# Kernel tuning notes

Hardware: AMD Instinct MI355X
Metric: run time of the kernel (lower is better)

The kernel has to match this reference:

```python
import jax, jax.numpy as jnp
import numpy as np

VEC_DIM = 300
NUM_DOCS = 500000
NUM_WORDS = 100000
BATCH = 4096
NUM_CTX = 10
NUM_NOISE_P1 = 26


def setup_inputs() -> dict:
    key = jax.random.key(0)
    k1, k2, k3, k4, k5 = jax.random.split(key, 5)
    context_ids = jax.random.randint(k1, (BATCH, NUM_CTX), 0, NUM_WORDS)
    doc_ids = jax.random.randint(k2, (BATCH,), 0, NUM_DOCS)
    target_noise_ids = jax.random.randint(k3, (BATCH, NUM_NOISE_P1), 0, NUM_WORDS)
    D = jax.random.normal(k4, (NUM_DOCS, VEC_DIM), dtype=jnp.float32)
    W = jax.random.normal(k5, (NUM_WORDS, VEC_DIM), dtype=jnp.float32)
    O = jnp.zeros((VEC_DIM, NUM_WORDS), dtype=jnp.float32)
    return {
        "context_ids": context_ids,
        "doc_ids": doc_ids,
        "target_noise_ids": target_noise_ids,
        "D": D,
        "W": W,
        "O": O,
    }


def reference(context_ids, doc_ids, target_noise_ids, D, W, O):
    # x[b] = D[doc_ids[b]] + sum_c W[context_ids[b, c]]   -> (B, vec_dim)
    x = D[doc_ids] + jnp.sum(W[context_ids], axis=1)
    # O[:, target_noise_ids] gathered as O.T[target_noise_ids] -> (B, N, vec_dim)
    # scores[b, n] = x[b] . O[:, target_noise_ids[b, n]]
    scores = jnp.einsum("bd,bnd->bn", x, O.T[target_noise_ids])
    return scores
```

## Files before the change

### kernel.cpp

```cpp
#include <hip/hip_runtime.h>

#define VEC_DIM   300
#define NUM_WORDS 100000
#define BATCH_N   4096
#define NUM_CTX   10
#define NUM_NOISE 26
#define TILE      64

__global__ __launch_bounds__(256) void transpose_kernel(
    const float* __restrict__ O,
    float*       __restrict__ OT)
{
    __shared__ float tile[TILE][TILE + 1];
    const int wBase = blockIdx.x * TILE;
    const int dBase = blockIdx.y * TILE;
    const int tx = threadIdx.x & (TILE - 1);
    const int ty = threadIdx.x >> 6;

    const int w_in = wBase + tx;
#pragma unroll
    for (int j = 0; j < TILE; j += 4) {
        const int d = dBase + ty + j;
        if (d < VEC_DIM && w_in < NUM_WORDS)
            tile[ty + j][tx] = O[(size_t)d * NUM_WORDS + w_in];
    }
    __syncthreads();

    const int d_out = dBase + tx;
#pragma unroll
    for (int j = 0; j < TILE; j += 4) {
        const int w = wBase + ty + j;
        if (w < NUM_WORDS && d_out < VEC_DIM)
            OT[(size_t)w * VEC_DIM + d_out] = tile[tx][ty + j];
    }
}

__global__ __launch_bounds__(256) void pvdm_score_kernel(
    const int*   __restrict__ context_ids,
    const int*   __restrict__ doc_ids,
    const int*   __restrict__ tn_ids,
    const float* __restrict__ D,
    const float* __restrict__ W,
    const float* __restrict__ OT,
    float*       __restrict__ out)
{
    __shared__ float xs[VEC_DIM];
    const int b   = blockIdx.x;
    const int tid = threadIdx.x;

    const int doc = doc_ids[b];
    int ctx[NUM_CTX];
#pragma unroll
    for (int c = 0; c < NUM_CTX; ++c) ctx[c] = context_ids[b * NUM_CTX + c];

    for (int d = tid; d < VEC_DIM; d += 256) {
        float v = D[(size_t)doc * VEC_DIM + d];
#pragma unroll
        for (int c = 0; c < NUM_CTX; ++c)
            v += W[(size_t)ctx[c] * VEC_DIM + d];
        xs[d] = v;
    }
    __syncthreads();

    const int wave = tid >> 6;
    const int lane = tid & 63;
    for (int n = wave; n < NUM_NOISE; n += 4) {
        const int t = tn_ids[b * NUM_NOISE + n];
        const float* row = OT + (size_t)t * VEC_DIM;
        float s = 0.0f;
        for (int d = lane; d < VEC_DIM; d += 64)
            s += xs[d] * row[d];
#pragma unroll
        for (int off = 32; off > 0; off >>= 1)
            s += __shfl_down(s, off, 64);
        if (lane == 0) out[b * NUM_NOISE + n] = s;
    }
}

__global__ __launch_bounds__(256) void pvdm_score_direct_kernel(
    const int*   __restrict__ context_ids,
    const int*   __restrict__ doc_ids,
    const int*   __restrict__ tn_ids,
    const float* __restrict__ D,
    const float* __restrict__ W,
    const float* __restrict__ O,
    float*       __restrict__ out)
{
    __shared__ float xs[VEC_DIM];
    const int b   = blockIdx.x;
    const int tid = threadIdx.x;
    const int doc = doc_ids[b];
    int ctx[NUM_CTX];
#pragma unroll
    for (int c = 0; c < NUM_CTX; ++c) ctx[c] = context_ids[b * NUM_CTX + c];
    for (int d = tid; d < VEC_DIM; d += 256) {
        float v = D[(size_t)doc * VEC_DIM + d];
#pragma unroll
        for (int c = 0; c < NUM_CTX; ++c)
            v += W[(size_t)ctx[c] * VEC_DIM + d];
        xs[d] = v;
    }
    __syncthreads();
    const int wave = tid >> 6;
    const int lane = tid & 63;
    for (int n = wave; n < NUM_NOISE; n += 4) {
        const int t = tn_ids[b * NUM_NOISE + n];
        float s = 0.0f;
        for (int d = lane; d < VEC_DIM; d += 64)
            s += xs[d] * O[(size_t)d * NUM_WORDS + t];
#pragma unroll
        for (int off = 32; off > 0; off >>= 1)
            s += __shfl_down(s, off, 64);
        if (lane == 0) out[b * NUM_NOISE + n] = s;
    }
}

extern "C" void kernel_launch(void* const* d_in, const int* in_sizes, int n_in,
                              void* d_out, int out_size, void* d_ws, size_t ws_size,
                              hipStream_t stream) {
    const int*   context_ids = (const int*)  d_in[0];
    const int*   doc_ids     = (const int*)  d_in[1];
    const int*   tn_ids      = (const int*)  d_in[2];
    const float* D           = (const float*)d_in[3];
    const float* W           = (const float*)d_in[4];
    const float* O           = (const float*)d_in[5];
    float*       out         = (float*)d_out;

    const size_t OT_BYTES = (size_t)NUM_WORDS * VEC_DIM * sizeof(float);

    if (ws_size >= OT_BYTES) {
        float* OT = (float*)d_ws;
        dim3 tgrid((NUM_WORDS + TILE - 1) / TILE, (VEC_DIM + TILE - 1) / TILE);
        transpose_kernel<<<tgrid, 256, 0, stream>>>(O, OT);
        pvdm_score_kernel<<<BATCH_N, 256, 0, stream>>>(
            context_ids, doc_ids, tn_ids, D, W, OT, out);
    } else {
        pvdm_score_direct_kernel<<<BATCH_N, 256, 0, stream>>>(
            context_ids, doc_ids, tn_ids, D, W, O, out);
    }
}
```

Measured before the change: 840.5 us.

## Vectorize transpose with full-row tiles and float4 score gathers

Rewrites the O transpose to load 32-word by full-dimension tiles with float4 reads and write whole contiguous OT rows with float4 stores. The score kernel now builds x with float4 loads using 75 threads and computes each dot product with float4 row reads, holding x in registers per lane. The aim is to cut transaction count and improve coalescing in the memory-bound transpose and gather. The larger shared tile reduces occupancy, and the strided shared-memory scatter may cause bank conflicts.

```diff
diff --git a/kernel.cpp b/kernel.cpp
--- a/kernel.cpp
+++ b/kernel.cpp
@@ -1,37 +1,38 @@
 #include <hip/hip_runtime.h>
 
 #define VEC_DIM   300
+#define VEC_F4    75
 #define NUM_WORDS 100000
 #define BATCH_N   4096
 #define NUM_CTX   10
 #define NUM_NOISE 26
-#define TILE      64
+#define TWORDS    32
 
 __global__ __launch_bounds__(256) void transpose_kernel(
     const float* __restrict__ O,
     float*       __restrict__ OT)
 {
-    __shared__ float tile[TILE][TILE + 1];
-    const int wBase = blockIdx.x * TILE;
-    const int dBase = blockIdx.y * TILE;
-    const int tx = threadIdx.x & (TILE - 1);
-    const int ty = threadIdx.x >> 6;
+    __shared__ float tile[TWORDS * VEC_DIM];
+    const int wBase = blockIdx.x * TWORDS;
+    const int tid   = threadIdx.x;
 
-    const int w_in = wBase + tx;
-#pragma unroll
-    for (int j = 0; j < TILE; j += 4) {
-        const int d = dBase + ty + j;
-        if (d < VEC_DIM && w_in < NUM_WORDS)
-            tile[ty + j][tx] = O[(size_t)d * NUM_WORDS + w_in];
+    for (int idx = tid; idx < VEC_DIM * (TWORDS / 4); idx += 256) {
+        const int d = idx >> 3;
+        const int c = idx & 7;
+        const float4 v = *reinterpret_cast<const float4*>(
+            O + (size_t)d * NUM_WORDS + wBase + 4 * c);
+        tile[(4 * c + 0) * VEC_DIM + d] = v.x;
+        tile[(4 * c + 1) * VEC_DIM + d] = v.y;
+        tile[(4 * c + 2) * VEC_DIM + d] = v.z;
+        tile[(4 * c + 3) * VEC_DIM + d] = v.w;
     }
     __syncthreads();
 
-    const int d_out = dBase + tx;
-#pragma unroll
-    for (int j = 0; j < TILE; j += 4) {
-        const int w = wBase + ty + j;
-        if (w < NUM_WORDS && d_out < VEC_DIM)
-            OT[(size_t)w * VEC_DIM + d_out] = tile[tx][ty + j];
+    for (int idx = tid; idx < TWORDS * VEC_F4; idx += 256) {
+        const int w = idx / VEC_F4;
+        const int c = idx - w * VEC_F4;
+        const float4 v = *reinterpret_cast<const float4*>(tile + w * VEC_DIM + 4 * c);
+        *reinterpret_cast<float4*>(OT + (size_t)(wBase + w) * VEC_DIM + 4 * c) = v;
     }
 }
 
@@ -44,36 +45,53 @@
     const float* __restrict__ OT,
     float*       __restrict__ out)
 {
-    __shared__ float xs[VEC_DIM];
+    __shared__ float4 xs4[VEC_F4];
     const int b   = blockIdx.x;
     const int tid = threadIdx.x;
 
-    const int doc = doc_ids[b];
-    int ctx[NUM_CTX];
+    if (tid < VEC_F4) {
+        const int doc = doc_ids[b];
+        const float4* __restrict__ Drow =
+            reinterpret_cast<const float4*>(D + (size_t)doc * VEC_DIM);
+        float4 v = Drow[tid];
 #pragma unroll
-    for (int c = 0; c < NUM_CTX; ++c) ctx[c] = context_ids[b * NUM_CTX + c];
-
-    for (int d = tid; d < VEC_DIM; d += 256) {
-        float v = D[(size_t)doc * VEC_DIM + d];
-#pragma unroll
-        for (int c = 0; c < NUM_CTX; ++c)
-            v += W[(size_t)ctx[c] * VEC_DIM + d];
-        xs[d] = v;
+        for (int c = 0; c < NUM_CTX; ++c) {
+            const int wd = context_ids[b * NUM_CTX + c];
+            const float4 u =
+                reinterpret_cast<const float4*>(W + (size_t)wd * VEC_DIM)[tid];
+            v.x += u.x; v.y += u.y; v.z += u.z; v.w += u.w;
+        }
+        xs4[tid] = v;
     }
     __syncthreads();
 
     const int wave = tid >> 6;
     const int lane = tid & 63;
-    for (int n = wave; n < NUM_NOISE; n += 4) {
-        const int t = tn_ids[b * NUM_NOISE + n];
-        const float* row = OT + (size_t)t * VEC_DIM;
-        float s = 0.0f;
-        for (int d = lane; d < VEC_DIM; d += 64)
-            s += xs[d] * row[d];
+
+    const float4 xa = xs4[lane];
+    float4 xb = make_float4(0.f, 0.f, 0.f, 0.f);
+    if (lane < VEC_F4 - 64) xb = xs4[64 + lane];
+
+    const int* __restrict__ tb = tn_ids + b * NUM_NOISE;
+
 #pragma unroll
-        for (int off = 32; off > 0; off >>= 1)
-            s += __shfl_down(s, off, 64);
-        if (lane == 0) out[b * NUM_NOISE + n] = s;
+    for (int k = 0; k < 7; ++k) {
+        const int n = wave + 4 * k;
+        if (n < NUM_NOISE) {
+            const int t = tb[n];
+            const float4* __restrict__ row =
+                reinterpret_cast<const float4*>(OT + (size_t)t * VEC_DIM);
+            const float4 ra = row[lane];
+            float s = ra.x * xa.x + ra.y * xa.y + ra.z * xa.z + ra.w * xa.w;
+            if (lane < VEC_F4 - 64) {
+                const float4 rb = row[64 + lane];
+                s += rb.x * xb.x + rb.y * xb.y + rb.z * xb.z + rb.w * xb.w;
+            }
+#pragma unroll
+            for (int off = 32; off > 0; off >>= 1)
+                s += __shfl_down(s, off, 64);
+            if (lane == 0) out[b * NUM_NOISE + n] = s;
+        }
     }
 }
 
@@ -130,8 +148,7 @@
 
     if (ws_size >= OT_BYTES) {
         float* OT = (float*)d_ws;
-        dim3 tgrid((NUM_WORDS + TILE - 1) / TILE, (VEC_DIM + TILE - 1) / TILE);
-        transpose_kernel<<<tgrid, 256, 0, stream>>>(O, OT);
+        transpose_kernel<<<NUM_WORDS / TWORDS, 256, 0, stream>>>(O, OT);
         pvdm_score_kernel<<<BATCH_N, 256, 0, stream>>>(
             context_ids, doc_ids, tn_ids, D, W, OT, out);
     } else {
```

Result: faster. 809.2 us (-3.7%).
